# Kernel tuning notes

Measured on AMD Instinct MI355X. Metric: run time of the kernel, lower is better.

The kernel has to match this reference:

```python
import jax, jax.numpy as jnp
import numpy as np

N_ATOMS = 10000
N_PAIR = 100000
F = 128
N_HEAD = 4
FH = F // N_HEAD  # 32
DEGREES = [1, 2, 3]
N_DEG = len(DEGREES)
REPEATS = np.array([2 * l + 1 for l in DEGREES])  # [3,5,7]
M_TOT = int(REPEATS.sum())  # 15
K_RBF = 32


def ssp(x):
    # shifted softplus: softplus(x) - log(2)
    return jax.nn.softplus(x) - jnp.log(2.0).astype(x.dtype)


def setup_inputs() -> dict:
    key = jax.random.key(0)
    ks = jax.random.split(key, 16)
    inp = {
        "x": jax.random.normal(ks[0], (N_ATOMS, F), jnp.float32),
        "rbf_ij": jax.random.normal(ks[1], (N_PAIR, K_RBF), jnp.float32),
        "sph_ij": jax.random.normal(ks[2], (N_PAIR, M_TOT), jnp.float32),
        "phi_r_cut": jax.random.uniform(ks[3], (N_PAIR,), jnp.float32),
        "idx_i": jnp.sort(jax.random.randint(ks[4], (N_PAIR,), 0, N_ATOMS)),
        "idx_j": jax.random.randint(ks[5], (N_PAIR,), 0, N_ATOMS),
        "pair_mask": jnp.ones((N_PAIR,), jnp.float32),
        # params
        "W_Q": jax.random.normal(ks[6], (N_DEG, N_HEAD, FH, FH), jnp.float32) / np.sqrt(FH),
        "W_K": jax.random.normal(ks[7], (N_DEG, N_HEAD, FH, FH), jnp.float32) / np.sqrt(FH),
        # in2f MLP: single dense F -> F
        "W_in": jax.random.normal(ks[8], (F, F), jnp.float32) / np.sqrt(F),
        "b_in": jnp.zeros((F,), jnp.float32),
        # radial filter MLP: K -> K (ssp) -> n_deg*F
        "W_f1": jax.random.normal(ks[9], (K_RBF, K_RBF), jnp.float32) / np.sqrt(K_RBF),
        "b_f1": jnp.zeros((K_RBF,), jnp.float32),
        "W_f2": jax.random.normal(ks[10], (K_RBF, N_DEG * F), jnp.float32) / np.sqrt(K_RBF),
        "b_f2": jnp.zeros((N_DEG * F,), jnp.float32),
        # f2out MLP: single dense F -> F
        "W_out": jax.random.normal(ks[11], (F, F), jnp.float32) / np.sqrt(F),
        "b_out": jnp.zeros((F,), jnp.float32),
    }
    return inp


def reference(x, rbf_ij, sph_ij, phi_r_cut, idx_i, idx_j, pair_mask,
              W_Q, W_K, W_in, b_in, W_f1, b_f1, W_f2, b_f2, W_out, b_out):
    n = x.shape[0]
    # in2f embedding (last in2f dim == F)
    x_f = x @ W_in + b_in                                  # (n, F)
    x_head = x_f.reshape(n, N_HEAD, FH)                    # (n, h, FH)

    # per-degree, per-head linear maps (the nested vmap matmuls)
    Q = jnp.einsum('dhij,nhj->ndhi', W_Q, x_head)          # (n, n_deg, h, FH)
    K = jnp.einsum('dhij,nhj->ndhi', W_K, x_head)

    m = pair_mask[:, None, None, None]
    Q_i = Q[idx_i] * m                                     # (P, n_deg, h, FH)
    K_j = K[idx_j] * m

    # radial filter: MLP(rbf) -> (P, n_deg, h, FH), scaled by cutoff
    h1 = ssp(rbf_ij @ W_f1 + b_f1)
    W_ij = (h1 @ W_f2 + b_f2).reshape(-1, N_DEG, N_HEAD, FH)
    W_ij = W_ij * phi_r_cut[:, None, None, None]

    # attention coefficients per degree/head
    alpha = jnp.sum(Q_i * K_j * W_ij, axis=-1)             # (P, n_deg, h)
    alpha = jnp.repeat(alpha, repeats=REPEATS, axis=1, total_repeat_length=M_TOT)  # (P, m_tot, h)
    alpha = alpha / jnp.sqrt(jnp.asarray(FH, x.dtype))     # att_scale

    # outer product of neighbor features with spherical harmonics
    x_j = x_head[idx_j] * pair_mask[:, None, None]         # (P, h, FH)
    z_ij = jnp.einsum('pm,phf->pmhf', sph_ij, x_j)         # (P, m_tot, h, FH)
    z_ij = alpha[:, :, :, None] * z_ij
    z_ij = z_ij.reshape(z_ij.shape[0], M_TOT, F)           # (P, m_tot, F)

    agg = jax.ops.segment_sum(z_ij, idx_i, num_segments=n)  # (n, m_tot, F)

    # f2out projection (last f2out dim == F)
    out = agg @ W_out + b_out                               # (n, m_tot, F)
    return out
```

## Files before the change

### kernel.cpp

```cpp
#include <hip/hip_runtime.h>
#include <hip/hip_bf16.h>

#define N_ATOMS 10000
#define N_PAIR  100000
#define F_DIM   128
#define N_HEAD  4
#define FH      32
#define N_DEG   3
#define M_TOT   15
#define K_RBF   32

typedef __attribute__((ext_vector_type(8))) short short8;
typedef __attribute__((ext_vector_type(4))) float f32x4;

union frag_cast { int i[4]; short8 s; };

__device__ __forceinline__ float sspf(float v) {
    float sp = fmaxf(v, 0.f) + log1pf(expf(-fabsf(v)));
    return sp - 0.69314718055994531f;
}

__device__ __forceinline__ unsigned short bf16_rne(float x) {
    unsigned int u = __float_as_uint(x);
    unsigned int r = u + 0x7fffu + ((u >> 16) & 1u);
    return (unsigned short)(r >> 16);
}
__device__ __forceinline__ float bf16_tof(unsigned short h) {
    return __uint_as_float(((unsigned int)h) << 16);
}

__global__ __launch_bounds__(256) void k_gemm128(
    const float* __restrict__ A, const float* __restrict__ B,
    const float* __restrict__ bias, float* __restrict__ C, int rows)
{
    __shared__ float As[32][132];
    __shared__ float Bs[32][132];
    int r0 = blockIdx.x * 128;
    int t = threadIdx.x;
    int ty = t >> 4, tx = t & 15;

    float acc[8][8];
    #pragma unroll
    for (int i = 0; i < 8; ++i)
        #pragma unroll
        for (int j = 0; j < 8; ++j) acc[i][j] = 0.f;

    for (int k0 = 0; k0 < 128; k0 += 32) {
        #pragma unroll
        for (int r = 0; r < 16; ++r) {
            int idx = t + 256 * r;
            int row = idx >> 5, kk = idx & 31;
            int grow = r0 + row;
            As[kk][row] = (grow < rows) ? A[grow * 128 + k0 + kk] : 0.f;
        }
        #pragma unroll
        for (int r = 0; r < 16; ++r) {
            int idx = t + 256 * r;
            int kk = idx >> 7, c = idx & 127;
            Bs[kk][c] = B[(k0 + kk) * 128 + c];
        }
        __syncthreads();

        #pragma unroll
        for (int kk = 0; kk < 32; ++kk) {
            float a[8], b[8];
            *(float4*)&a[0] = *(const float4*)&As[kk][ty * 4];
            *(float4*)&a[4] = *(const float4*)&As[kk][64 + ty * 4];
            *(float4*)&b[0] = *(const float4*)&Bs[kk][tx * 4];
            *(float4*)&b[4] = *(const float4*)&Bs[kk][64 + tx * 4];
            #pragma unroll
            for (int i = 0; i < 8; ++i)
                #pragma unroll
                for (int j = 0; j < 8; ++j)
                    acc[i][j] = fmaf(a[i], b[j], acc[i][j]);
        }
        __syncthreads();
    }

    float bj[8];
    #pragma unroll
    for (int j = 0; j < 4; ++j) { bj[j] = bias[tx * 4 + j]; bj[4 + j] = bias[64 + tx * 4 + j]; }

    #pragma unroll
    for (int i = 0; i < 8; ++i) {
        int row = r0 + ((i < 4) ? (ty * 4 + i) : (64 + ty * 4 + (i - 4)));
        if (row < rows) {
            float4 v0, v1;
            v0.x = acc[i][0] + bj[0]; v0.y = acc[i][1] + bj[1];
            v0.z = acc[i][2] + bj[2]; v0.w = acc[i][3] + bj[3];
            v1.x = acc[i][4] + bj[4]; v1.y = acc[i][5] + bj[5];
            v1.z = acc[i][6] + bj[6]; v1.w = acc[i][7] + bj[7];
            *(float4*)&C[row * 128 + tx * 4] = v0;
            *(float4*)&C[row * 128 + 64 + tx * 4] = v1;
        }
    }
}

__global__ __launch_bounds__(384) void k_qk(
    const float* __restrict__ xh, const float* __restrict__ W_Q,
    const float* __restrict__ W_K, float* __restrict__ Q, float* __restrict__ K)
{
    __shared__ float xfs[32][128];
    int t = threadIdx.x;
    int h = (t >> 5) & 3;
    float wq[32], wk[32];
    const float4* wqp = (const float4*)(W_Q + t * 32);
    const float4* wkp = (const float4*)(W_K + t * 32);
    #pragma unroll
    for (int j4 = 0; j4 < 8; ++j4) {
        float4 a = wqp[j4], b = wkp[j4];
        wq[4 * j4 + 0] = a.x; wq[4 * j4 + 1] = a.y; wq[4 * j4 + 2] = a.z; wq[4 * j4 + 3] = a.w;
        wk[4 * j4 + 0] = b.x; wk[4 * j4 + 1] = b.y; wk[4 * j4 + 2] = b.z; wk[4 * j4 + 3] = b.w;
    }
    int ab = blockIdx.x * 32;
    for (int idx = t; idx < 4096; idx += 384) {
        int aa = idx >> 7, f = idx & 127;
        int ag = ab + aa;
        xfs[aa][f] = (ag < N_ATOMS) ? xh[ag * 128 + f] : 0.f;
    }
    __syncthreads();
    for (int aa = 0; aa < 32; ++aa) {
        int ag = ab + aa;
        if (ag >= N_ATOMS) break;
        const float4* xv = (const float4*)&xfs[aa][h * 32];
        float q0 = 0.f, q1 = 0.f, k0 = 0.f, k1 = 0.f;
        #pragma unroll
        for (int j4 = 0; j4 < 8; j4 += 2) {
            float4 x0 = xv[j4], x1 = xv[j4 + 1];
            q0 = fmaf(wq[4 * j4 + 0], x0.x, q0); q0 = fmaf(wq[4 * j4 + 1], x0.y, q0);
            q0 = fmaf(wq[4 * j4 + 2], x0.z, q0); q0 = fmaf(wq[4 * j4 + 3], x0.w, q0);
            q1 = fmaf(wq[4 * j4 + 4], x1.x, q1); q1 = fmaf(wq[4 * j4 + 5], x1.y, q1);
            q1 = fmaf(wq[4 * j4 + 6], x1.z, q1); q1 = fmaf(wq[4 * j4 + 7], x1.w, q1);
            k0 = fmaf(wk[4 * j4 + 0], x0.x, k0); k0 = fmaf(wk[4 * j4 + 1], x0.y, k0);
            k0 = fmaf(wk[4 * j4 + 2], x0.z, k0); k0 = fmaf(wk[4 * j4 + 3], x0.w, k0);
            k1 = fmaf(wk[4 * j4 + 4], x1.x, k1); k1 = fmaf(wk[4 * j4 + 5], x1.y, k1);
            k1 = fmaf(wk[4 * j4 + 6], x1.z, k1); k1 = fmaf(wk[4 * j4 + 7], x1.w, k1);
        }
        Q[ag * 384 + t] = q0 + q1;
        K[ag * 384 + t] = k0 + k1;
    }
}

__global__ __launch_bounds__(256) void k_cvt_w2(
    const float* __restrict__ W, unsigned short* __restrict__ Wh,
    unsigned short* __restrict__ Wl)
{
    int idx = blockIdx.x * 256 + threadIdx.x;
    if (idx < 12288) {
        int e = idx >> 5, k = idx & 31;
        float v = W[k * 384 + e];
        unsigned short h = bf16_rne(v);
        unsigned short l = bf16_rne(v - bf16_tof(h));
        Wh[e * 32 + k] = h;
        Wl[e * 32 + k] = l;
    }
}

__global__ __launch_bounds__(256) void k_pair(
    const float* __restrict__ rbf, const float* __restrict__ phi,
    const float* __restrict__ mask, const int* __restrict__ idx_i,
    const int* __restrict__ idx_j, const float* __restrict__ W_f1,
    const float* __restrict__ b_f1, const unsigned short* __restrict__ W2h,
    const unsigned short* __restrict__ W2l, const float* __restrict__ b_f2,
    const float* __restrict__ Q, const float* __restrict__ K,
    float* __restrict__ alpha)
{
    __shared__ float g_s[16][388];
    __shared__ unsigned int h1p_s[16][36];
    __shared__ int   i_s[16];
    __shared__ int   j_s[16];
    __shared__ float phim_s[16];

    float (*rbf_s)[33] = (float (*)[33])(&g_s[0][0]);
    float (*wf1_s)[33] = (float (*)[33])(&g_s[0][0] + 16 * 33);

    int t = threadIdx.x;
    int p0 = blockIdx.x * 16;

    for (int idx = t; idx < 1536; idx += 256) {
        if (idx < 512) {
            rbf_s[idx >> 5][idx & 31] = rbf[p0 * 32 + idx];
        } else {
            int k = idx - 512;
            wf1_s[k >> 5][k & 31] = W_f1[k];
        }
    }
    if (t < 16) {
        int pg = p0 + t;
        i_s[t] = idx_i[pg];
        j_s[t] = idx_j[pg];
        float m = mask[pg];
        phim_s[t] = phi[pg] * m * m * 0.17677669529663687f;
    }
    __syncthreads();

    {
        int p = t >> 4, c0 = (t & 15) * 2;
        float acc0 = b_f1[c0], acc1 = b_f1[c0 + 1];
        #pragma unroll
        for (int k = 0; k < 32; ++k) {
            float rv = rbf_s[p][k];
            acc0 = fmaf(rv, wf1_s[k][c0], acc0);
            acc1 = fmaf(rv, wf1_s[k][c0 + 1], acc1);
        }
        float h0 = sspf(acc0), h1v = sspf(acc1);
        unsigned short hh0 = bf16_rne(h0);
        unsigned short ll0 = bf16_rne(h0 - bf16_tof(hh0));
        unsigned short hh1 = bf16_rne(h1v);
        unsigned short ll1 = bf16_rne(h1v - bf16_tof(hh1));
        h1p_s[p][c0]     = ((unsigned int)hh0 << 16) | (unsigned int)ll0;
        h1p_s[p][c0 + 1] = ((unsigned int)hh1 << 16) | (unsigned int)ll1;
    }
    __syncthreads();

    #pragma unroll
    for (int it = 0; it < 6; ++it) {
        int idx = it * 256 + t;
        int p = idx / 96;
        int c4 = idx - p * 96;
        const float4* qp = (const float4*)(Q + i_s[p] * 384) + c4;
        const float4* kp = (const float4*)(K + j_s[p] * 384) + c4;
        float4 qv = *qp, kv = *kp;
        float4 gv;
        gv.x = qv.x * kv.x; gv.y = qv.y * kv.y;
        gv.z = qv.z * kv.z; gv.w = qv.w * kv.w;
        *(float4*)&g_s[p][c4 * 4] = gv;
    }
    __syncthreads();

    int wave = t >> 6, lane = t & 63;
    int quad = lane >> 4, l15 = lane & 15;

    short8 ah, al;
    {
        const unsigned int* hp = &h1p_s[l15][quad * 8];
        uint4 u01 = *(const uint4*)hp;
        uint4 u23 = *(const uint4*)(hp + 4);
        unsigned int u[8] = {u01.x, u01.y, u01.z, u01.w, u23.x, u23.y, u23.z, u23.w};
        frag_cast fh, fl;
        #pragma unroll
        for (int q = 0; q < 4; ++q) {
            unsigned int a0 = u[2 * q], a1 = u[2 * q + 1];
            fh.i[q] = (int)((a0 >> 16) | (a1 & 0xffff0000u));
            fl.i[q] = (int)((a0 & 0xffffu) | (a1 << 16));
        }
        ah = fh.s;
        al = fl.s;
    }

    #pragma unroll
    for (int dd = 0; dd < 3; ++dd) {
        int dh = wave * 3 + dd;
        int e_base = dh * 32;
        short8 bh0 = *(const short8*)(W2h + (e_base + l15) * 32 + quad * 8);
        short8 bl0 = *(const short8*)(W2l + (e_base + l15) * 32 + quad * 8);
        short8 bh1 = *(const short8*)(W2h + (e_base + 16 + l15) * 32 + quad * 8);
        short8 bl1 = *(const short8*)(W2l + (e_base + 16 + l15) * 32 + quad * 8);
        float b2v0 = b_f2[e_base + l15];
        float b2v1 = b_f2[e_base + 16 + l15];

        f32x4 s0 = {0.f, 0.f, 0.f, 0.f};
        f32x4 s1 = {0.f, 0.f, 0.f, 0.f};
        s0 = __builtin_amdgcn_mfma_f32_16x16x32_bf16(ah, bh0, s0, 0, 0, 0);
        s1 = __builtin_amdgcn_mfma_f32_16x16x32_bf16(ah, bh1, s1, 0, 0, 0);
        s0 = __builtin_amdgcn_mfma_f32_16x16x32_bf16(al, bh0, s0, 0, 0, 0);
        s1 = __builtin_amdgcn_mfma_f32_16x16x32_bf16(al, bh1, s1, 0, 0, 0);
        s0 = __builtin_amdgcn_mfma_f32_16x16x32_bf16(ah, bl0, s0, 0, 0, 0);
        s1 = __builtin_amdgcn_mfma_f32_16x16x32_bf16(ah, bl1, s1, 0, 0, 0);

        float vsum[4];
        #pragma unroll
        for (int r = 0; r < 4; ++r) {
            int prow = quad * 4 + r;
            float v = (s0[r] + b2v0) * g_s[prow][e_base + l15]
                    + (s1[r] + b2v1) * g_s[prow][e_base + 16 + l15];
            #pragma unroll
            for (int off = 8; off >= 1; off >>= 1)
                v += __shfl_xor(v, off, 16);
            vsum[r] = v;
        }
        if (l15 == 0) {
            #pragma unroll
            for (int r = 0; r < 4; ++r) {
                int prow = quad * 4 + r;
                alpha[(p0 + prow) * 12 + dh] = vsum[r] * phim_s[prow];
            }
        }
    }
}

__device__ __forceinline__ int lower_bound_i(const int* __restrict__ arr, int n, int val) {
    int lo = 0, hi = n;
    while (lo < hi) {
        int mid = (lo + hi) >> 1;
        if (arr[mid] < val) lo = mid + 1; else hi = mid;
    }
    return lo;
}

__global__ __launch_bounds__(256) void k_seg(const int* __restrict__ idx_i,
                                             int* __restrict__ seg)
{
    int a = blockIdx.x * 256 + threadIdx.x;
    if (a <= N_ATOMS) seg[a] = lower_bound_i(idx_i, N_PAIR, a);
}

__global__ __launch_bounds__(256) void k_cvt_b(
    const float* __restrict__ W, unsigned short* __restrict__ Bth,
    unsigned short* __restrict__ Btl)
{
    int idx = blockIdx.x * 256 + threadIdx.x;
    int cc = idx >> 7, kk = idx & 127;
    float v = W[kk * 128 + cc];
    unsigned short h = bf16_rne(v);
    unsigned short l = bf16_rne(v - bf16_tof(h));
    Bth[cc * 128 + kk] = h;
    Btl[cc * 128 + kk] = l;
}

__global__ __launch_bounds__(512) void k_agg_out(
    const float* __restrict__ xh, const float* __restrict__ alpha,
    const float* __restrict__ sph, const int* __restrict__ seg,
    const int* __restrict__ idx_j, const float* __restrict__ mask,
    const unsigned short* __restrict__ Bth, const unsigned short* __restrict__ Btl,
    const float* __restrict__ bias, float* __restrict__ C)
{
    __shared__ float red_s[2][15][132];
    __shared__ unsigned int ap_s[2][16][132];

    int tid = threadIdx.x;
    int sub = tid >> 8;
    int t   = tid & 127;
    int grp = (tid >> 7) & 1;
    int a = blockIdx.x * 2 + sub;
    int h = t >> 5;
    int lo = seg[a], hi = seg[a + 1];

    float acc[15];
    #pragma unroll
    for (int m = 0; m < 15; ++m) acc[m] = 0.f;

    int p = lo + grp;
    float x_cur = 0.f;
    if (p < hi) x_cur = xh[idx_j[p] * 128 + t];
    for (; p < hi; p += 2) {
        int pn = p + 2;
        float x_nxt = 0.f;
        if (pn < hi) x_nxt = xh[idx_j[pn] * 128 + t];
        float xj = x_cur * mask[p];
        float a0v = alpha[p * 12 + h];
        float a1v = alpha[p * 12 + 4 + h];
        float a2v = alpha[p * 12 + 8 + h];
        const float* sp = sph + p * 15;
        #pragma unroll
        for (int m = 0; m < 15; ++m) {
            float al = (m < 3) ? a0v : ((m < 8) ? a1v : a2v);
            acc[m] = fmaf(sp[m] * al, xj, acc[m]);
        }
        x_cur = x_nxt;
    }

    if (grp == 1) {
        #pragma unroll
        for (int m = 0; m < 15; ++m) red_s[sub][m][t] = acc[m];
    }
    __syncthreads();
    if (grp == 0) {
        #pragma unroll
        for (int m = 0; m < 15; ++m) {
            float v = acc[m] + red_s[sub][m][t];
            unsigned short hh = bf16_rne(v);
            unsigned short ll = bf16_rne(v - bf16_tof(hh));
            ap_s[sub][m][t] = ((unsigned int)hh << 16) | (unsigned int)ll;
        }
        ap_s[sub][15][t] = 0u;
    }
    __syncthreads();

    int wave = tid >> 6, lane = tid & 63;
    int quad = lane >> 4, l15 = lane & 15;
    int am = wave >> 2;
    int cb = (wave & 3) * 32;
    long ga = (long)blockIdx.x * 2 + am;

    short8 ah[4], al[4];
    #pragma unroll
    for (int ks = 0; ks < 4; ++ks) {
        const unsigned int* hp = &ap_s[am][l15][ks * 32 + quad * 8];
        uint4 u01 = *(const uint4*)hp;
        uint4 u23 = *(const uint4*)(hp + 4);
        unsigned int u[8] = {u01.x, u01.y, u01.z, u01.w, u23.x, u23.y, u23.z, u23.w};
        frag_cast fh, fl;
        #pragma unroll
        for (int q = 0; q < 4; ++q) {
            unsigned int a0 = u[2 * q], a1 = u[2 * q + 1];
            fh.i[q] = (int)((a0 >> 16) | (a1 & 0xffff0000u));
            fl.i[q] = (int)((a0 & 0xffffu) | (a1 << 16));
        }
        ah[ks] = fh.s;
        al[ks] = fl.s;
    }

    #pragma unroll
    for (int ct = 0; ct < 2; ++ct) {
        int c = cb + ct * 16;
        short8 bh[4], bl[4];
        #pragma unroll
        for (int ks = 0; ks < 4; ++ks) {
            int off = (c + l15) * 128 + ks * 32 + quad * 8;
            bh[ks] = *(const short8*)(Bth + off);
            bl[ks] = *(const short8*)(Btl + off);
        }
        f32x4 oacc = {0.f, 0.f, 0.f, 0.f};
        #pragma unroll
        for (int ks = 0; ks < 4; ++ks) {
            oacc = __builtin_amdgcn_mfma_f32_16x16x32_bf16(ah[ks], bh[ks], oacc, 0, 0, 0);
            oacc = __builtin_amdgcn_mfma_f32_16x16x32_bf16(al[ks], bh[ks], oacc, 0, 0, 0);
            oacc = __builtin_amdgcn_mfma_f32_16x16x32_bf16(ah[ks], bl[ks], oacc, 0, 0, 0);
        }
        float bv = bias[c + l15];
        #pragma unroll
        for (int r = 0; r < 4; ++r) {
            int row = quad * 4 + r;
            if (row < 15)
                C[(ga * 15 + row) * 128 + c + l15] = oacc[r] + bv;
        }
    }
}

extern "C" void kernel_launch(void* const* d_in, const int* in_sizes, int n_in,
                              void* d_out, int out_size, void* d_ws, size_t ws_size,
                              hipStream_t stream) {
    const float* x        = (const float*)d_in[0];
    const float* rbf_ij   = (const float*)d_in[1];
    const float* sph_ij   = (const float*)d_in[2];
    const float* phi_r    = (const float*)d_in[3];
    const int*   idx_i    = (const int*)d_in[4];
    const int*   idx_j    = (const int*)d_in[5];
    const float* pmask    = (const float*)d_in[6];
    const float* W_Q      = (const float*)d_in[7];
    const float* W_K      = (const float*)d_in[8];
    const float* W_in     = (const float*)d_in[9];
    const float* b_in     = (const float*)d_in[10];
    const float* W_f1     = (const float*)d_in[11];
    const float* b_f1     = (const float*)d_in[12];
    const float* W_f2     = (const float*)d_in[13];
    const float* b_f2     = (const float*)d_in[14];
    const float* W_out    = (const float*)d_in[15];
    const float* b_out    = (const float*)d_in[16];
    float* out = (float*)d_out;

    float* ws    = (float*)d_ws;
    float* xh    = ws;
    float* Qbuf  = xh + N_ATOMS * F_DIM;
    float* Kbuf  = Qbuf + N_ATOMS * 384;
    float* alpha = Kbuf + N_ATOMS * 384;
    int*   seg   = (int*)(alpha + N_PAIR * 12);
    unsigned short* Bth = (unsigned short*)(seg + 10432);
    unsigned short* Btl = Bth + 16384;
    unsigned short* W2h = Btl + 16384;
    unsigned short* W2l = W2h + 12288;

    k_seg<<<(N_ATOMS + 256) / 256, 256, 0, stream>>>(idx_i, seg);
    k_cvt_b<<<64, 256, 0, stream>>>(W_out, Bth, Btl);
    k_cvt_w2<<<48, 256, 0, stream>>>(W_f2, W2h, W2l);
    k_gemm128<<<(N_ATOMS + 127) / 128, 256, 0, stream>>>(x, W_in, b_in, xh, N_ATOMS);
    k_qk<<<(N_ATOMS + 31) / 32, 384, 0, stream>>>(xh, W_Q, W_K, Qbuf, Kbuf);
    k_pair<<<N_PAIR / 16, 256, 0, stream>>>(rbf_ij, phi_r, pmask, idx_i, idx_j,
                                            W_f1, b_f1, W2h, W2l, b_f2,
                                            Qbuf, Kbuf, alpha);
    k_agg_out<<<N_ATOMS / 2, 512, 0, stream>>>(xh, alpha, sph_ij, seg, idx_j, pmask,
                                               Bth, Btl, b_out, out);
}
```

Measured before the change: 391.5 us.

## Assign one atom per block with four pair groups and deeper prefetch

The aggregation kernel now gives each 512-thread block a single atom instead of two. Its four 128-thread groups each take every fourth pair and reduce through shared memory. The pair loop software-pipelines the next pair's x row, mask, alpha and spherical-harmonic values, and prefetches idx_j two steps ahead, to hide gather latency. Each of the eight waves then computes one 16-column MFMA tile of the output projection. This raises parallelism per atom and the number of blocks, but adds reduction traffic and register pressure, and atoms with few pairs leave groups idle.

Result: faster. 365.8 us (-6.6%).

```diff
diff --git a/kernel.cpp b/kernel.cpp
--- a/kernel.cpp
+++ b/kernel.cpp
@@ -325,14 +325,13 @@
     const unsigned short* __restrict__ Bth, const unsigned short* __restrict__ Btl,
     const float* __restrict__ bias, float* __restrict__ C)
 {
-    __shared__ float red_s[2][15][132];
-    __shared__ unsigned int ap_s[2][16][132];
+    __shared__ float red_s[3][15][132];
+    __shared__ unsigned int ap_s[16][132];
 
     int tid = threadIdx.x;
-    int sub = tid >> 8;
     int t   = tid & 127;
-    int grp = (tid >> 7) & 1;
-    int a = blockIdx.x * 2 + sub;
+    int grp = tid >> 7;
+    int a = blockIdx.x;
     int h = t >> 5;
     int lo = seg[a], hi = seg[a + 1];
 
@@ -341,52 +340,76 @@
     for (int m = 0; m < 15; ++m) acc[m] = 0.f;
 
     int p = lo + grp;
-    float x_cur = 0.f;
-    if (p < hi) x_cur = xh[idx_j[p] * 128 + t];
-    for (; p < hi; p += 2) {
-        int pn = p + 2;
-        float x_nxt = 0.f;
-        if (pn < hi) x_nxt = xh[idx_j[pn] * 128 + t];
-        float xj = x_cur * mask[p];
-        float a0v = alpha[p * 12 + h];
-        float a1v = alpha[p * 12 + 4 + h];
-        float a2v = alpha[p * 12 + 8 + h];
-        const float* sp = sph + p * 15;
+    float x_c = 0.f, m_c = 0.f, a_c0 = 0.f, a_c1 = 0.f, a_c2 = 0.f;
+    float s_c[15];
+    int jn = 0;
+    if (p < hi) {
+        int j0 = idx_j[p];
+        m_c  = mask[p];
+        a_c0 = alpha[p * 12 + h];
+        a_c1 = alpha[p * 12 + 4 + h];
+        a_c2 = alpha[p * 12 + 8 + h];
+        #pragma unroll
+        for (int m = 0; m < 15; ++m) s_c[m] = sph[p * 15 + m];
+        x_c = xh[j0 * 128 + t];
+        if (p + 4 < hi) jn = idx_j[p + 4];
+    }
+
+    while (p < hi) {
+        int pn = p + 4;
+        float x_n = 0.f, m_n = 0.f, an0 = 0.f, an1 = 0.f, an2 = 0.f;
+        float s_n[15];
+        #pragma unroll
+        for (int m = 0; m < 15; ++m) s_n[m] = 0.f;
+        int jn2 = 0;
+        if (pn < hi) {
+            x_n = xh[jn * 128 + t];
+            m_n = mask[pn];
+            an0 = alpha[pn * 12 + h];
+            an1 = alpha[pn * 12 + 4 + h];
+            an2 = alpha[pn * 12 + 8 + h];
+            #pragma unroll
+            for (int m = 0; m < 15; ++m) s_n[m] = sph[pn * 15 + m];
+            if (pn + 4 < hi) jn2 = idx_j[pn + 4];
+        }
+        float xj = x_c * m_c;
         #pragma unroll
         for (int m = 0; m < 15; ++m) {
-            float al = (m < 3) ? a0v : ((m < 8) ? a1v : a2v);
-            acc[m] = fmaf(sp[m] * al, xj, acc[m]);
-        }
-        x_cur = x_nxt;
-    }
-
-    if (grp == 1) {
-        #pragma unroll
-        for (int m = 0; m < 15; ++m) red_s[sub][m][t] = acc[m];
+            float av = (m < 3) ? a_c0 : ((m < 8) ? a_c1 : a_c2);
+            acc[m] = fmaf(s_c[m] * av, xj, acc[m]);
+        }
+        x_c = x_n; m_c = m_n; a_c0 = an0; a_c1 = an1; a_c2 = an2;
+        #pragma unroll
+        for (int m = 0; m < 15; ++m) s_c[m] = s_n[m];
+        jn = jn2;
+        p = pn;
+    }
+
+    if (grp >= 1) {
+        #pragma unroll
+        for (int m = 0; m < 15; ++m) red_s[grp - 1][m][t] = acc[m];
     }
     __syncthreads();
     if (grp == 0) {
         #pragma unroll
         for (int m = 0; m < 15; ++m) {
-            float v = acc[m] + red_s[sub][m][t];
+            float v = acc[m] + red_s[0][m][t] + red_s[1][m][t] + red_s[2][m][t];
             unsigned short hh = bf16_rne(v);
             unsigned short ll = bf16_rne(v - bf16_tof(hh));
-            ap_s[sub][m][t] = ((unsigned int)hh << 16) | (unsigned int)ll;
-        }
-        ap_s[sub][15][t] = 0u;
+            ap_s[m][t] = ((unsigned int)hh << 16) | (unsigned int)ll;
+        }
+        ap_s[15][t] = 0u;
     }
     __syncthreads();
 
     int wave = tid >> 6, lane = tid & 63;
     int quad = lane >> 4, l15 = lane & 15;
-    int am = wave >> 2;
-    int cb = (wave & 3) * 32;
-    long ga = (long)blockIdx.x * 2 + am;
-
-    short8 ah[4], al[4];
+    int c = wave * 16;
+
+    short8 fa_h[4], fa_l[4];
     #pragma unroll
     for (int ks = 0; ks < 4; ++ks) {
-        const unsigned int* hp = &ap_s[am][l15][ks * 32 + quad * 8];
+        const unsigned int* hp = &ap_s[l15][ks * 32 + quad * 8];
         uint4 u01 = *(const uint4*)hp;
         uint4 u23 = *(const uint4*)(hp + 4);
         unsigned int u[8] = {u01.x, u01.y, u01.z, u01.w, u23.x, u23.y, u23.z, u23.w};
@@ -397,34 +420,30 @@
             fh.i[q] = (int)((a0 >> 16) | (a1 & 0xffff0000u));
             fl.i[q] = (int)((a0 & 0xffffu) | (a1 << 16));
         }
-        ah[ks] = fh.s;
-        al[ks] = fl.s;
-    }
-
-    #pragma unroll
-    for (int ct = 0; ct < 2; ++ct) {
-        int c = cb + ct * 16;
-        short8 bh[4], bl[4];
-        #pragma unroll
-        for (int ks = 0; ks < 4; ++ks) {
-            int off = (c + l15) * 128 + ks * 32 + quad * 8;
-            bh[ks] = *(const short8*)(Bth + off);
-            bl[ks] = *(const short8*)(Btl + off);
-        }
-        f32x4 oacc = {0.f, 0.f, 0.f, 0.f};
-        #pragma unroll
-        for (int ks = 0; ks < 4; ++ks) {
-            oacc = __builtin_amdgcn_mfma_f32_16x16x32_bf16(ah[ks], bh[ks], oacc, 0, 0, 0);
-            oacc = __builtin_amdgcn_mfma_f32_16x16x32_bf16(al[ks], bh[ks], oacc, 0, 0, 0);
-            oacc = __builtin_amdgcn_mfma_f32_16x16x32_bf16(ah[ks], bl[ks], oacc, 0, 0, 0);
-        }
-        float bv = bias[c + l15];
-        #pragma unroll
-        for (int r = 0; r < 4; ++r) {
-            int row = quad * 4 + r;
-            if (row < 15)
-                C[(ga * 15 + row) * 128 + c + l15] = oacc[r] + bv;
-        }
+        fa_h[ks] = fh.s;
+        fa_l[ks] = fl.s;
+    }
+
+    short8 bh[4], bl[4];
+    #pragma unroll
+    for (int ks = 0; ks < 4; ++ks) {
+        int off = (c + l15) * 128 + ks * 32 + quad * 8;
+        bh[ks] = *(const short8*)(Bth + off);
+        bl[ks] = *(const short8*)(Btl + off);
+    }
+    f32x4 oacc = {0.f, 0.f, 0.f, 0.f};
+    #pragma unroll
+    for (int ks = 0; ks < 4; ++ks) {
+        oacc = __builtin_amdgcn_mfma_f32_16x16x32_bf16(fa_h[ks], bh[ks], oacc, 0, 0, 0);
+        oacc = __builtin_amdgcn_mfma_f32_16x16x32_bf16(fa_l[ks], bh[ks], oacc, 0, 0, 0);
+        oacc = __builtin_amdgcn_mfma_f32_16x16x32_bf16(fa_h[ks], bl[ks], oacc, 0, 0, 0);
+    }
+    float bv = bias[c + l15];
+    #pragma unroll
+    for (int r = 0; r < 4; ++r) {
+        int row = quad * 4 + r;
+        if (row < 15)
+            C[((long)a * 15 + row) * 128 + c + l15] = oacc[r] + bv;
     }
 }
 
@@ -469,6 +488,6 @@
     k_pair<<<N_PAIR / 16, 256, 0, stream>>>(rbf_ij, phi_r, pmask, idx_i, idx_j,
                                             W_f1, b_f1, W2h, W2l, b_f2,
                                             Qbuf, Kbuf, alpha);
-    k_agg_out<<<N_ATOMS / 2, 512, 0, stream>>>(xh, alpha, sph_ij, seg, idx_j, pmask,
-                                               Bth, Btl, b_out, out);
-}
+    k_agg_out<<<N_ATOMS, 512, 0, stream>>>(xh, alpha, sph_ij, seg, idx_j, pmask,
+                                           Bth, Btl, b_out, out);
+}
```
